# Optimization experiments

Measured on AMD Instinct MI355X. Metric: run time of the kernel, lower is better.

Reference implementation:

```python
import jax, jax.numpy as jnp
import numpy as np

N = 100000
E = 1600000
F = 64
THETA = (0.6, -0.4, 0.3, -0.2, 0.1)  # k = 5 polynomial coefficients


def setup_inputs() -> dict:
    key = jax.random.key(0)
    kx, ke = jax.random.split(key)
    x = jax.random.normal(kx, (N, F), dtype=jnp.float32)
    edge_index = jax.random.randint(ke, (2, E), 0, N, dtype=jnp.int64)
    return {"x": x, "edge_index": edge_index}


def _l_sym_mul(feat, src, dst, deg_inv_sqrt, n):
    # L_sym * feat = feat - D^{-1/2} A D^{-1/2} feat
    src_norm = feat[src] * deg_inv_sqrt[src]            # [E, F] gather + scale
    agg = jax.ops.segment_sum(src_norm, dst, num_segments=n)  # scatter-add to dst
    return feat - deg_inv_sqrt * agg


def reference(x, edge_index):
    src, dst = edge_index[0], edge_index[1]
    n = x.shape[0]
    # in-degree from dst, clamp to >= 1, D^{-1/2} as [N, 1]
    deg = jax.ops.segment_sum(jnp.ones((src.shape[0],), dtype=x.dtype), dst,
                              num_segments=n)
    deg = jnp.maximum(deg, 1.0)[:, None]
    deg_inv_sqrt = deg ** -0.5

    h_acc = THETA[0] * x
    feat = x
    for k in range(1, len(THETA)):
        feat = _l_sym_mul(feat, src, dst, deg_inv_sqrt, n)
        h_acc = h_acc + THETA[k] * feat
    return h_acc
```

## Files before the change

### kernel.cpp

```cpp
#include <hip/hip_runtime.h>
#include <hip/hip_fp16.h>


constexpr int kF = 64;
constexpr int BSHIFT = 8;
constexpr int NB = 1 << BSHIFT;
constexpr int TILE = 2048;
constexpr int KMAX = 512;

typedef unsigned nv4u __attribute__((ext_vector_type(4)));
typedef float    nv4f __attribute__((ext_vector_type(4)));

static __device__ __forceinline__ float hlo(unsigned u) {
    return __half2float(__ushort_as_half((unsigned short)(u & 0xffffu)));
}
static __device__ __forceinline__ float hhi(unsigned u) {
    return __half2float(__ushort_as_half((unsigned short)(u >> 16)));
}
static __device__ __forceinline__ unsigned pack2h(float a, float b) {
    return (unsigned)__half_as_ushort(__float2half_rn(a)) |
           ((unsigned)__half_as_ushort(__float2half_rn(b)) << 16);
}
static __device__ __forceinline__ unsigned padd2(unsigned a, unsigned b) {
    __half2 ha = *reinterpret_cast<__half2*>(&a);
    __half2 hb = *reinterpret_cast<__half2*>(&b);
    __half2 hc = __hadd2(ha, hb);
    return *reinterpret_cast<unsigned*>(&hc);
}

__global__ void k_binA(const int* __restrict__ src, const int* __restrict__ dst,
                       unsigned* __restrict__ pairs, int* __restrict__ gcursor,
                       const float4* __restrict__ x4, uint4* __restrict__ xb4,
                       int n8, int E, int K, int cap) {
    __shared__ int hist[KMAX];
    __shared__ int gb[KMAX];
    const int tid = threadIdx.x;
    const long long tb = (long long)blockIdx.x * TILE;
    const int tcount = (int)min((long long)TILE, (long long)E - tb);

    {
        int per = (n8 + gridDim.x - 1) / (int)gridDim.x;
        int b0 = blockIdx.x * per;
        int b1 = min(b0 + per, n8);
        for (int i = b0 + tid; i < b1; i += 512) {
            float4 a = x4[2 * i];
            float4 b = x4[2 * i + 1];
            uint4 o;
            o.x = pack2h(a.x, a.y);
            o.y = pack2h(a.z, a.w);
            o.z = pack2h(b.x, b.y);
            o.w = pack2h(b.z, b.w);
            xb4[i] = o;
        }
    }

    hist[tid] = 0;
    __syncthreads();
    int dc[4], sc[4];
    #pragma unroll
    for (int k = 0; k < 4; ++k) {
        int i = tid + k * 512;
        if (i < tcount) {
            dc[k] = dst[tb + i];
            sc[k] = src[tb + i];
            atomicAdd(&hist[dc[k] >> BSHIFT], 1);
        } else {
            dc[k] = -1;
        }
    }
    __syncthreads();
    int hv = hist[tid];
    gb[tid] = (tid < K && hv > 0) ? atomicAdd(&gcursor[tid], hv) : 0;
    hist[tid] = 0;
    __syncthreads();
    #pragma unroll
    for (int k = 0; k < 4; ++k) {
        if (dc[k] >= 0) {
            int d = dc[k];
            int b = d >> BSHIFT;
            int pos = atomicAdd(&hist[b], 1);
            pairs[(size_t)b * cap + gb[b] + pos] =
                ((unsigned)(d & (NB - 1)) << 23) | (unsigned)sc[k];
        }
    }
}

__global__ void k_binB(const unsigned* __restrict__ pairs, const int* __restrict__ gcursor,
                       int* __restrict__ rp, float* __restrict__ dinv2,
                       float* __restrict__ rdeg, int* __restrict__ csr,
                       int* __restrict__ csr0,
                       const uint4* __restrict__ xb, uint4* __restrict__ g0,
                       int N, int E, int K, int cap) {
    __shared__ int gsc[KMAX];
    __shared__ int cnt[NB];
    __shared__ int stmp[NB];
    __shared__ int cur[NB];
    __shared__ float sdinv[NB];
    const int b = blockIdx.x;
    const int tid = threadIdx.x;

    if (b == 0 && tid < 8)
        g0[((size_t)N << 3) + tid] = make_uint4(0, 0, 0, 0);

    int gv = (tid < K) ? gcursor[tid] : 0;
    gsc[tid] = gv;
    __syncthreads();
    for (int o = 1; o < KMAX; o <<= 1) {
        int t = (tid >= o) ? gsc[tid - o] : 0;
        __syncthreads();
        gsc[tid] += t;
        __syncthreads();
    }
    const int ecnt = gcursor[b];
    const int base = gsc[b] - ecnt;
    const unsigned* bp = pairs + (size_t)b * cap;

    if (tid < NB) cnt[tid] = 0;
    __syncthreads();
    for (int i = tid; i < ecnt; i += 512)
        atomicAdd(&cnt[bp[i] >> 23], 1);
    __syncthreads();
    int v = (tid < NB) ? cnt[tid] : 0;
    if (tid < NB) stmp[tid] = v;
    __syncthreads();
    for (int o = 1; o < NB; o <<= 1) {
        int t = (tid >= o && tid < NB) ? stmp[tid - o] : 0;
        __syncthreads();
        if (tid < NB) stmp[tid] += t;
        __syncthreads();
    }
    int node = (b << BSHIFT) + tid;
    if (tid < NB) {
        int abs0 = base + stmp[tid] - v;
        cur[tid] = abs0;
        float d = fmaxf((float)v, 1.0f);
        sdinv[tid] = rsqrtf(d);
        if (node < N) {
            rp[node] = abs0;
            dinv2[node] = 1.0f / d;
            rdeg[node]  = sqrtf(d);
        }
    }
    if (b == K - 1 && tid == 0) rp[N] = E;
    __syncthreads();
    for (int i = tid; i < ecnt; i += 512) {
        unsigned p = bp[i];
        int pos = atomicAdd(&cur[p >> 23], 1);
        csr[pos] = (int)(p & 0x7FFFFFu);
    }
    __syncthreads();
    if (tid < NB && node < N) {
        int abs0 = base + stmp[tid] - v;
        int4 q0, q1;
        q0.x = (0 < v) ? csr[abs0 + 0] : N;
        q0.y = (1 < v) ? csr[abs0 + 1] : N;
        q0.z = (2 < v) ? csr[abs0 + 2] : N;
        q0.w = (3 < v) ? csr[abs0 + 3] : N;
        q1.x = (4 < v) ? csr[abs0 + 4] : N;
        q1.y = (5 < v) ? csr[abs0 + 5] : N;
        q1.z = (6 < v) ? csr[abs0 + 6] : N;
        q1.w = (7 < v) ? csr[abs0 + 7] : N;
        *(int4*)(csr0 + ((size_t)node << 3))     = q0;
        *(int4*)(csr0 + ((size_t)node << 3) + 4) = q1;
    }
    const int nbase = b << BSHIFT;
    const int qmax = min(NB, N - nbase) << 3;
    const uint4* xbp = xb + ((size_t)nbase << 3);
    uint4* g0p = g0 + ((size_t)nbase << 3);
    for (int q = tid; q < qmax; q += 512) {
        float di = sdinv[q >> 3];
        uint4 xv = xbp[q];
        uint4 o;
        o.x = pack2h(di * hlo(xv.x), di * hhi(xv.x));
        o.y = pack2h(di * hlo(xv.y), di * hhi(xv.y));
        o.z = pack2h(di * hlo(xv.z), di * hhi(xv.z));
        o.w = pack2h(di * hlo(xv.w), di * hhi(xv.w));
        g0p[q] = o;
    }
}

template <bool LAST>
__global__ void k_gather(const int* __restrict__ rp, const int* __restrict__ csr,
                         const int* __restrict__ csr0,
                         const unsigned short* __restrict__ gin,
                         const float* __restrict__ dinv2,
                         unsigned short* __restrict__ gout,
                         const unsigned short* __restrict__ xb,
                         const unsigned short* __restrict__ g1t,
                         const unsigned short* __restrict__ g2t,
                         const float* __restrict__ rdeg,
                         float* __restrict__ h, int n,
                         float t0, float t1, float t2, float t3, float t4) {
    if (!LAST && blockIdx.x == 0 && threadIdx.x < 8)
        *(((uint4*)(gout + ((size_t)n << 6))) + threadIdx.x) = make_uint4(0, 0, 0, 0);

    int wid = (blockIdx.x * blockDim.x + threadIdx.x) >> 6;
    int lane = threadIdx.x & 63;
    int half = lane >> 5;
    int r = (lane >> 3) & 3;
    int c = lane & 7;
    int node = wid * 2 + half;
    if (wid * 2 >= n) return;
    bool valid = node < n;

    int s1 = n, s2 = n;
    if (valid) {
        s1 = csr0[((size_t)node << 3) + r];
        s2 = csr0[((size_t)node << 3) + r + 4];
    }
    int beg = valid ? rp[node] : 0;
    int end = valid ? rp[node + 1] : 0;

    const bool ep = (r == 0) && valid;
    size_t off = ((size_t)node << 6) + (c << 3);
    uint4 rr = make_uint4(0, 0, 0, 0);
    float d2 = 0.f, rd = 0.f;
    nv4u xv = {0u, 0u, 0u, 0u}, aa = {0u, 0u, 0u, 0u}, bb = {0u, 0u, 0u, 0u};
    if (ep) {
        rr = *(const uint4*)(gin + off);
        d2 = dinv2[node];
        if (LAST) {
            xv = __builtin_nontemporal_load((const nv4u*)(xb + off));
            aa = __builtin_nontemporal_load((const nv4u*)(g1t + off));
            bb = __builtin_nontemporal_load((const nv4u*)(g2t + off));
            rd = rdeg[node];
        }
    }

    int len = end - beg;
    int olen = __shfl_xor(len, 32, 64);
    int mlen = (len > olen) ? len : olen;

    unsigned acc[4] = {0u, 0u, 0u, 0u};

    uint4 rc1 = *(const uint4*)(gin + ((size_t)s1 << 6) + (c << 3));
    uint4 rc2 = *(const uint4*)(gin + ((size_t)s2 << 6) + (c << 3));
    int sn1 = n, sn2 = n;
    {
        int j1b = beg + 8 + r, j2b = j1b + 4;
        bool vb = 8 < mlen;
        bool b1 = vb && (j1b < end), b2 = vb && (j2b < end);
        sn1 = csr[b1 ? j1b : 0]; sn1 = b1 ? sn1 : n;
        sn2 = csr[b2 ? j2b : 0]; sn2 = b2 ? sn2 : n;
    }
    for (int i = 0; i < mlen; i += 8) {
        uint4 rn1 = *(const uint4*)(gin + ((size_t)sn1 << 6) + (c << 3));
        uint4 rn2 = *(const uint4*)(gin + ((size_t)sn2 << 6) + (c << 3));
        int j1n = beg + i + 16 + r, j2n = j1n + 4;
        bool vn = (i + 16) < mlen;
        bool t1c = vn && (j1n < end), t2c = vn && (j2n < end);
        int st1 = csr[t1c ? j1n : 0]; st1 = t1c ? st1 : n;
        int st2 = csr[t2c ? j2n : 0]; st2 = t2c ? st2 : n;
        acc[0] = padd2(acc[0], rc1.x); acc[1] = padd2(acc[1], rc1.y);
        acc[2] = padd2(acc[2], rc1.z); acc[3] = padd2(acc[3], rc1.w);
        acc[0] = padd2(acc[0], rc2.x); acc[1] = padd2(acc[1], rc2.y);
        acc[2] = padd2(acc[2], rc2.z); acc[3] = padd2(acc[3], rc2.w);
        rc1 = rn1; rc2 = rn2;
        sn1 = st1; sn2 = st2;
    }
    #pragma unroll
    for (int m = 8; m <= 16; m <<= 1) {
        #pragma unroll
        for (int i = 0; i < 4; ++i)
            acc[i] = padd2(acc[i], __shfl_xor(acc[i], m, 64));
    }

    if (ep) {
        float v[8];
        v[0] = hlo(rr.x) - d2 * hlo(acc[0]); v[1] = hhi(rr.x) - d2 * hhi(acc[0]);
        v[2] = hlo(rr.y) - d2 * hlo(acc[1]); v[3] = hhi(rr.y) - d2 * hhi(acc[1]);
        v[4] = hlo(rr.z) - d2 * hlo(acc[2]); v[5] = hhi(rr.z) - d2 * hhi(acc[2]);
        v[6] = hlo(rr.w) - d2 * hlo(acc[3]); v[7] = hhi(rr.w) - d2 * hhi(acc[3]);
        if (!LAST) {
            nv4u o;
            o.x = pack2h(v[0], v[1]);
            o.y = pack2h(v[2], v[3]);
            o.z = pack2h(v[4], v[5]);
            o.w = pack2h(v[6], v[7]);
            __builtin_nontemporal_store(o, (nv4u*)(gout + off));
        } else {
            float s1f = rd * t1, s2f = rd * t2, s3f = rd * t3, s4f = rd * t4;
            nv4f h0, h1;
            h0.x = t0 * hlo(xv.x) + s1f * hlo(aa.x) + s2f * hlo(bb.x) + s3f * hlo(rr.x) + s4f * v[0];
            h0.y = t0 * hhi(xv.x) + s1f * hhi(aa.x) + s2f * hhi(bb.x) + s3f * hhi(rr.x) + s4f * v[1];
            h0.z = t0 * hlo(xv.y) + s1f * hlo(aa.y) + s2f * hlo(bb.y) + s3f * hlo(rr.y) + s4f * v[2];
            h0.w = t0 * hhi(xv.y) + s1f * hhi(aa.y) + s2f * hhi(bb.y) + s3f * hhi(rr.y) + s4f * v[3];
            h1.x = t0 * hlo(xv.z) + s1f * hlo(aa.z) + s2f * hlo(bb.z) + s3f * hlo(rr.z) + s4f * v[4];
            h1.y = t0 * hhi(xv.z) + s1f * hhi(aa.z) + s2f * hhi(bb.z) + s3f * hhi(rr.z) + s4f * v[5];
            h1.z = t0 * hlo(xv.w) + s1f * hlo(aa.w) + s2f * hlo(bb.w) + s3f * hlo(rr.w) + s4f * v[6];
            h1.w = t0 * hhi(xv.w) + s1f * hhi(aa.w) + s2f * hhi(bb.w) + s3f * hhi(rr.w) + s4f * v[7];
            __builtin_nontemporal_store(h0, (nv4f*)(h + off));
            __builtin_nontemporal_store(h1, (nv4f*)(h + off + 4));
        }
    }
}

extern "C" void kernel_launch(void* const* d_in, const int* in_sizes, int n_in,
                              void* d_out, int out_size, void* d_ws, size_t ws_size,
                              hipStream_t stream) {
    const float* x  = (const float*)d_in[0];
    const int*   ei = (const int*)d_in[1];
    const int N = in_sizes[0] / kF;
    const int E = in_sizes[1] / 2;
    const int* src = ei;
    const int* dst = ei + E;
    float* h = (float*)d_out;

    const int K = (N + NB - 1) >> BSHIFT;
    const int cap = 2 * ((E + K - 1) / K);

    char* ws = (char*)d_ws;
    size_t off = 0;
    auto carve = [&](size_t bytes) {
        void* p = ws + off;
        off = (off + bytes + 511) & ~(size_t)511;
        return p;
    };
    size_t gbytes = (size_t)(N + 1) * kF * 2;
    int*            gcursor = (int*)carve((size_t)KMAX * 4);
    int*            rp      = (int*)carve((size_t)(N + 1) * 4);
    float*          dinv2   = (float*)carve((size_t)N * 4);
    float*          rdeg    = (float*)carve((size_t)N * 4);
    int*            csr     = (int*)carve((size_t)E * 4);
    int*            csr0    = (int*)carve((size_t)N * 8 * 4);
    unsigned short* xb      = (unsigned short*)carve((size_t)N * kF * 2);
    unsigned short* g0      = (unsigned short*)carve(gbytes);
    size_t pbytes = (size_t)K * cap * 4;
    unsigned short* g1      = (unsigned short*)carve(gbytes > pbytes ? gbytes : pbytes);
    unsigned short* g2      = (unsigned short*)carve(gbytes);
    unsigned short* g3      = (unsigned short*)carve(gbytes);
    unsigned*       pairs   = (unsigned*)g1;

    const float theta[5] = {0.6f, -0.4f, 0.3f, -0.2f, 0.1f};
    const int n8 = N * kF / 8;

    hipMemsetAsync(gcursor, 0, (size_t)KMAX * 4, stream);
    k_binA<<<(E + TILE - 1) / TILE, 512, 0, stream>>>(src, dst, pairs, gcursor,
                                                      (const float4*)x, (uint4*)xb,
                                                      n8, E, K, cap);
    k_binB<<<K, 512, 0, stream>>>(pairs, gcursor, rp, dinv2, rdeg, csr, csr0,
                                  (const uint4*)xb, (uint4*)g0, N, E, K, cap);

    const int nwaves = (N + 1) / 2;
    const int gblocks = (nwaves + 3) / 4;
    k_gather<false><<<gblocks, 256, 0, stream>>>(rp, csr, csr0, g0, dinv2, g1,
                                                 nullptr, nullptr, nullptr, nullptr,
                                                 nullptr, N, 0, 0, 0, 0, 0);
    k_gather<false><<<gblocks, 256, 0, stream>>>(rp, csr, csr0, g1, dinv2, g2,
                                                 nullptr, nullptr, nullptr, nullptr,
                                                 nullptr, N, 0, 0, 0, 0, 0);
    k_gather<false><<<gblocks, 256, 0, stream>>>(rp, csr, csr0, g2, dinv2, g3,
                                                 nullptr, nullptr, nullptr, nullptr,
                                                 nullptr, N, 0, 0, 0, 0, 0);
    k_gather<true><<<gblocks, 256, 0, stream>>>(rp, csr, csr0, g3, dinv2, nullptr,
                                                xb, g1, g2, rdeg, h, N,
                                                theta[0], theta[1], theta[2],
                                                theta[3], theta[4]);
}
```

Measured before the change: 243.2 us.

## Stage binned edge pairs in shared memory for coalesced scatter writes

The binning kernel now handles 8192 edges per block instead of 2048. Each block runs a prefix scan over its per-bucket histogram, places the packed pairs into LDS sorted by bucket, and then writes each bucket's run to global memory contiguously instead of scattering them. The goal is fewer scattered global writes and fewer global atomics per edge. The cost is more shared memory, more registers for 16 edges per thread, a 9-step scan with barriers, and only about 196 blocks, which may underfill the GPU and spread the x-to-fp16 conversion over fewer blocks.

```diff
diff --git a/kernel.cpp b/kernel.cpp
--- a/kernel.cpp
+++ b/kernel.cpp
@@ -5,7 +5,7 @@
 constexpr int kF = 64;
 constexpr int BSHIFT = 8;
 constexpr int NB = 1 << BSHIFT;
-constexpr int TILE = 2048;
+constexpr int TILEA = 8192;
 constexpr int KMAX = 512;
 
 typedef unsigned nv4u __attribute__((ext_vector_type(4)));
@@ -32,11 +32,14 @@
                        unsigned* __restrict__ pairs, int* __restrict__ gcursor,
                        const float4* __restrict__ x4, uint4* __restrict__ xb4,
                        int n8, int E, int K, int cap) {
+    __shared__ unsigned stage[TILEA];
+    __shared__ unsigned short stageB[TILEA];
     __shared__ int hist[KMAX];
+    __shared__ int lb[KMAX];
     __shared__ int gb[KMAX];
     const int tid = threadIdx.x;
-    const long long tb = (long long)blockIdx.x * TILE;
-    const int tcount = (int)min((long long)TILE, (long long)E - tb);
+    const long long tb = (long long)blockIdx.x * TILEA;
+    const int tcount = (int)min((long long)TILEA, (long long)E - tb);
 
     {
         int per = (n8 + gridDim.x - 1) / (int)gridDim.x;
@@ -56,9 +59,9 @@
 
     hist[tid] = 0;
     __syncthreads();
-    int dc[4], sc[4];
+    int dc[16], sc[16];
     #pragma unroll
-    for (int k = 0; k < 4; ++k) {
+    for (int k = 0; k < 16; ++k) {
         int i = tid + k * 512;
         if (i < tcount) {
             dc[k] = dst[tb + i];
@@ -69,19 +72,35 @@
         }
     }
     __syncthreads();
-    int hv = hist[tid];
-    gb[tid] = (tid < K && hv > 0) ? atomicAdd(&gcursor[tid], hv) : 0;
-    hist[tid] = 0;
+    const int cnt = hist[tid];
+    lb[tid] = cnt;
+    __syncthreads();
+    for (int o = 1; o < KMAX; o <<= 1) {
+        int t = (tid >= o) ? lb[tid - o] : 0;
+        __syncthreads();
+        lb[tid] += t;
+        __syncthreads();
+    }
+    const int excl = lb[tid] - cnt;
+    __syncthreads();
+    lb[tid] = excl;
+    gb[tid] = (tid < K && cnt > 0) ? atomicAdd(&gcursor[tid], cnt) : 0;
+    hist[tid] = excl;
     __syncthreads();
     #pragma unroll
-    for (int k = 0; k < 4; ++k) {
+    for (int k = 0; k < 16; ++k) {
         if (dc[k] >= 0) {
             int d = dc[k];
             int b = d >> BSHIFT;
             int pos = atomicAdd(&hist[b], 1);
-            pairs[(size_t)b * cap + gb[b] + pos] =
-                ((unsigned)(d & (NB - 1)) << 23) | (unsigned)sc[k];
-        }
+            stage[pos]  = ((unsigned)(d & (NB - 1)) << 23) | (unsigned)sc[k];
+            stageB[pos] = (unsigned short)b;
+        }
+    }
+    __syncthreads();
+    for (int j = tid; j < tcount; j += 512) {
+        int b = stageB[j];
+        pairs[(size_t)b * cap + gb[b] + (j - lb[b])] = stage[j];
     }
 }
 
@@ -335,9 +354,9 @@
     const int n8 = N * kF / 8;
 
     hipMemsetAsync(gcursor, 0, (size_t)KMAX * 4, stream);
-    k_binA<<<(E + TILE - 1) / TILE, 512, 0, stream>>>(src, dst, pairs, gcursor,
-                                                      (const float4*)x, (uint4*)xb,
-                                                      n8, E, K, cap);
+    k_binA<<<(E + TILEA - 1) / TILEA, 512, 0, stream>>>(src, dst, pairs, gcursor,
+                                                        (const float4*)x, (uint4*)xb,
+                                                        n8, E, K, cap);
     k_binB<<<K, 512, 0, stream>>>(pairs, gcursor, rp, dinv2, rdeg, csr, csr0,
                                   (const uint4*)xb, (uint4*)g0, N, E, K, cap);
 
```

Measured after the change: 237.7 us. -2.2%, faster.
